# Kernel tuning notes

Hardware: AMD Instinct MI355X
Metric: run time of the kernel (lower is better)

Reference implementation:

```python
import jax, jax.numpy as jnp
import numpy as np

ALPHA = 0.25
GAMMA = 2.0
EPS = 1e-4


def calc_iou(a, b):
    # a: [A,4] anchors xyxy, b: [M,4] gt boxes xyxy -> [A,M]
    area = (b[:, 2] - b[:, 0]) * (b[:, 3] - b[:, 1])  # [M]
    iw = jnp.minimum(a[:, 2:3], b[None, :, 2]) - jnp.maximum(a[:, 0:1], b[None, :, 0])
    ih = jnp.minimum(a[:, 3:4], b[None, :, 3]) - jnp.maximum(a[:, 1:2], b[None, :, 1])
    iw = jnp.clip(iw, 0.0)
    ih = jnp.clip(ih, 0.0)
    anchor_area = ((a[:, 2] - a[:, 0]) * (a[:, 3] - a[:, 1]))[:, None]
    ua = jnp.clip(anchor_area + area[None, :] - iw * ih, 1e-8)
    return iw * ih / ua


def setup_inputs() -> dict:
    B, A, K, M = 8, 120000, 80, 32
    key = jax.random.key(0)
    k1, k2, k3, k4, k5, k6, k7 = jax.random.split(key, 7)
    classifications = jax.random.uniform(k1, (B, A, K), dtype=jnp.float32)
    regressions = jax.random.normal(k2, (B, A, 4), dtype=jnp.float32) * 0.1
    # anchors: valid xyxy boxes with positive width/height
    a_xy = jax.random.uniform(k3, (A, 2), minval=0.0, maxval=480.0)
    a_wh = jax.random.uniform(k4, (A, 2), minval=16.0, maxval=128.0)
    anchors = jnp.concatenate([a_xy, a_xy + a_wh], axis=1)[None].astype(jnp.float32)
    # annotations: [B, M, 5] valid gt boxes, labels in [0, K)
    g_xy = jax.random.uniform(k5, (B, M, 2), minval=0.0, maxval=400.0)
    g_wh = jax.random.uniform(k6, (B, M, 2), minval=20.0, maxval=120.0)
    labels = jax.random.randint(k7, (B, M, 1), 0, K).astype(jnp.float32)
    annotations = jnp.concatenate([g_xy, g_xy + g_wh, labels], axis=2).astype(jnp.float32)
    return {"classifications": classifications, "regressions": regressions,
            "anchors": anchors, "annotations": annotations}


def reference(classifications, regressions, anchors, annotations):
    anchor = anchors[0]  # [A,4]
    aw = anchor[:, 2] - anchor[:, 0]
    ah = anchor[:, 3] - anchor[:, 1]
    acx = anchor[:, 0] + 0.5 * aw
    acy = anchor[:, 1] + 0.5 * ah
    reg_scale = jnp.array([0.1, 0.1, 0.2, 0.2], dtype=classifications.dtype)

    def per_item(cls, reg, ann):
        # cls: [A,K], reg: [A,4], ann: [M,5]
        valid = ann[:, 4] != -1.0  # [M] padding mask
        c = jnp.clip(cls, EPS, 1.0 - EPS)
        iou = jnp.where(valid[None, :], calc_iou(anchor, ann[:, :4]), -1.0)  # [A,M]
        iou_max = iou.max(axis=1)
        iou_argmax = iou.argmax(axis=1)
        assigned = ann[iou_argmax]  # [A,5] gather
        pos = iou_max >= 0.5
        neg = iou_max < 0.4
        num_pos = pos.sum().astype(c.dtype)
        # targets: 1 at assigned class for positives, 0 for negatives, -1 = ignore
        onehot = jax.nn.one_hot(assigned[:, 4].astype(jnp.int32), c.shape[1], dtype=c.dtype)
        t = jnp.where(pos[:, None], onehot, jnp.where(neg[:, None], 0.0, -1.0))
        alpha_factor = jnp.where(t == 1.0, ALPHA, 1.0 - ALPHA)
        focal_weight = jnp.where(t == 1.0, 1.0 - c, c)
        bce = -(t * jnp.log(c) + (1.0 - t) * jnp.log(1.0 - c))
        cls_loss = jnp.where(t != -1.0, alpha_factor * focal_weight ** GAMMA * bce, 0.0)
        cls_loss = cls_loss.sum() / jnp.maximum(num_pos, 1.0)
        gw0 = assigned[:, 2] - assigned[:, 0]
        gh0 = assigned[:, 3] - assigned[:, 1]
        gcx = assigned[:, 0] + 0.5 * gw0
        gcy = assigned[:, 1] + 0.5 * gh0
        gw = jnp.maximum(gw0, 1.0)
        gh = jnp.maximum(gh0, 1.0)
        rt = jnp.stack([(gcx - acx) / aw, (gcy - acy) / ah,
                        jnp.log(gw / aw), jnp.log(gh / ah)], axis=1) / reg_scale
        diff = jnp.abs(rt - reg)
        smooth = jnp.where(diff <= 1.0 / 9.0, 0.5 * 9.0 * diff ** 2, diff - 0.5 / 9.0)
        reg_loss = jnp.where(num_pos > 0.0,
                             (smooth * pos[:, None]).sum() / jnp.maximum(num_pos * 4.0, 1.0),
                             0.0)
        return cls_loss, reg_loss

    cls_l, reg_l = jax.vmap(per_item)(classifications, regressions, annotations)
    return cls_l.mean(keepdims=True), reg_l.mean(keepdims=True)
```

## Files before the change

### kernel.cpp

```cpp
#include <hip/hip_runtime.h>

#define NB 8
#define NA 120000
#define NK 80
#define NM 32

#define ALPHA_F 0.25f
#define EPS_F 1e-4f

#define TPB (NA / 64)
#define BLKW 4
#define BPBW ((TPB + BLKW - 1) / BLKW)


typedef float f32x4 __attribute__((ext_vector_type(4)));

__device__ __forceinline__ f32x4 ntload4(const f32x4* p) {
    return __builtin_nontemporal_load(p);
}

__device__ __forceinline__ float clampc(float x) {
    return fminf(fmaxf(x, EPS_F), 1.0f - EPS_F);
}
__device__ __forceinline__ float negl(float c) {
    return (1.0f - ALPHA_F) * c * c * (-__logf(1.0f - c));
}
__device__ __forceinline__ float posl(float c) {
    const float omc = 1.0f - c;
    return ALPHA_F * omc * omc * (-__logf(c));
}
__device__ __forceinline__ float negl4v(f32x4 v) {
    return negl(clampc(v.x)) + negl(clampc(v.y)) + negl(clampc(v.z)) + negl(clampc(v.w));
}

__global__ __launch_bounds__(256) void fused_kernel(
    const float* __restrict__ anchors,
    const float* __restrict__ regressions,
    const float* __restrict__ annotations,
    const float* __restrict__ cls,
    float* __restrict__ part)
{
    const int b = blockIdx.x / BPBW;
    const int blk = blockIdx.x % BPBW;
    const int wid = threadIdx.x >> 6;
    const int lane = threadIdx.x & 63;
    const int tile = blk * BLKW + wid;

    __shared__ float ann[NM * 5];
    __shared__ float barea[NM];
    if (threadIdx.x < NM * 5) ann[threadIdx.x] = annotations[b * NM * 5 + threadIdx.x];
    __syncthreads();
    if (threadIdx.x < NM) {
        const float* r = &ann[threadIdx.x * 5];
        barea[threadIdx.x] = (r[2] - r[0]) * (r[3] - r[1]);
    }
    __syncthreads();

    float reg_local = 0.0f;
    float pos_local = 0.0f;
    float cls_local = 0.0f;

    if (tile < TPB) {
        const int a = tile * 64 + lane;
        float maskf = 1.0f;

        {
            const float4 av = ((const float4*)anchors)[a];
            const float aw = av.z - av.x;
            const float ah = av.w - av.y;
            const float aarea = aw * ah;

            float bi = -1.0f, bu = 1.0f;
            int bm = 0;
            #pragma unroll 4
            for (int m = 0; m < NM; ++m) {
                const float bx1 = ann[m * 5 + 0];
                const float by1 = ann[m * 5 + 1];
                const float bx2 = ann[m * 5 + 2];
                const float by2 = ann[m * 5 + 3];
                const float lbl = ann[m * 5 + 4];
                const float iw = fmaxf(fminf(av.z, bx2) - fmaxf(av.x, bx1), 0.0f);
                const float ih = fmaxf(fminf(av.w, by2) - fmaxf(av.y, by1), 0.0f);
                float inter = iw * ih;
                float ua = fmaxf(aarea + barea[m] - inter, 1e-8f);
                if (lbl == -1.0f) { inter = -1.0f; ua = 1.0f; }
                if (inter * bu > bi * ua) { bi = inter; bu = ua; bm = m; }
            }

            if (bi >= 0.5f * bu) {
                const int st = (int)ann[bm * 5 + 4];
                const float bx1 = ann[bm * 5 + 0];
                const float by1 = ann[bm * 5 + 1];
                const float bx2 = ann[bm * 5 + 2];
                const float by2 = ann[bm * 5 + 3];
                const float gw0 = bx2 - bx1;
                const float gh0 = by2 - by1;
                const float gcx = bx1 + 0.5f * gw0;
                const float gcy = by1 + 0.5f * gh0;
                const float gw = fmaxf(gw0, 1.0f);
                const float gh = fmaxf(gh0, 1.0f);
                const float acx = av.x + 0.5f * aw;
                const float acy = av.y + 0.5f * ah;
                const float rt0 = ((gcx - acx) / aw) / 0.1f;
                const float rt1 = ((gcy - acy) / ah) / 0.1f;
                const float rt2 = logf(gw / aw) / 0.2f;
                const float rt3 = logf(gh / ah) / 0.2f;
                const float4 rg = ((const float4*)regressions)[b * NA + a];
                float s = 0.0f, d;
                d = fabsf(rt0 - rg.x); s += (d <= 1.0f / 9.0f) ? 4.5f * d * d : d - 0.5f / 9.0f;
                d = fabsf(rt1 - rg.y); s += (d <= 1.0f / 9.0f) ? 4.5f * d * d : d - 0.5f / 9.0f;
                d = fabsf(rt2 - rg.z); s += (d <= 1.0f / 9.0f) ? 4.5f * d * d : d - 0.5f / 9.0f;
                d = fabsf(rt3 - rg.w); s += (d <= 1.0f / 9.0f) ? 4.5f * d * d : d - 0.5f / 9.0f;
                reg_local = s;
                pos_local = 1.0f;
                const float c = clampc(cls[((size_t)b * NA + a) * NK + st]);
                cls_local = posl(c) - negl(c);
            } else if (bi >= 0.4f * bu) {
                maskf = 0.0f;
            }
        }

        unsigned long long ig = __ballot(maskf == 0.0f);

        const f32x4* __restrict__ p =
            (const f32x4*)(cls + ((size_t)b * NA + (size_t)tile * 64) * NK);
        float sum = 0.0f;
        #pragma unroll
        for (int o = 0; o < 4; ++o) {
            f32x4 v[5];
            #pragma unroll
            for (int u = 0; u < 5; ++u)
                v[u] = ntload4(p + (o * 5 + u) * 64 + lane);
            #pragma unroll
            for (int u = 0; u < 5; ++u)
                sum += negl4v(v[u]);
        }

        while (ig) {
            const int r = __ffsll(ig) - 1;
            ig &= ig - 1;
            if (lane < 20)
                sum -= negl4v(ntload4(p + r * 20 + lane));
        }
        cls_local += sum;
    }

    #pragma unroll
    for (int o = 32; o > 0; o >>= 1) {
        cls_local += __shfl_down(cls_local, o, 64);
        reg_local += __shfl_down(reg_local, o, 64);
        pos_local += __shfl_down(pos_local, o, 64);
    }
    __shared__ float wc[BLKW], wr[BLKW], wp[BLKW];
    if (lane == 0) { wc[wid] = cls_local; wr[wid] = reg_local; wp[wid] = pos_local; }
    __syncthreads();
    if (threadIdx.x == 0) {
        float csum = 0.0f, rsum = 0.0f, psum = 0.0f;
        #pragma unroll
        for (int i = 0; i < BLKW; ++i) { csum += wc[i]; rsum += wr[i]; psum += wp[i]; }
        float4 o4;
        o4.x = csum; o4.y = rsum; o4.z = psum; o4.w = 0.0f;
        ((float4*)part)[blockIdx.x] = o4;
    }
}

__global__ __launch_bounds__(512) void finalize_kernel(
    const float* __restrict__ part,
    float* __restrict__ out)
{
    __shared__ float redC[NB], redR[NB], redP[NB];
    const int w = threadIdx.x >> 6;
    const int lane = threadIdx.x & 63;

    float c = 0.0f, r = 0.0f, p = 0.0f;
    #pragma unroll
    for (int u = 0; u < 8; ++u) {
        const int i = u * 64 + lane;
        if (i < BPBW) {
            const float4 q = ((const float4*)part)[w * BPBW + i];
            c += q.x; r += q.y; p += q.z;
        }
    }
    #pragma unroll
    for (int o = 32; o > 0; o >>= 1) {
        c += __shfl_down(c, o, 64);
        r += __shfl_down(r, o, 64);
        p += __shfl_down(p, o, 64);
    }
    if (lane == 0) { redC[w] = c; redR[w] = r; redP[w] = p; }
    __syncthreads();
    if (threadIdx.x == 0) {
        float cs = 0.0f, rs = 0.0f;
        #pragma unroll
        for (int b = 0; b < NB; ++b) {
            const float P = redP[b];
            cs += redC[b] / fmaxf(P, 1.0f);
            rs += (P > 0.0f) ? redR[b] / fmaxf(P * 4.0f, 1.0f) : 0.0f;
        }
        out[0] = cs / (float)NB;
        out[1] = rs / (float)NB;
    }
}

extern "C" void kernel_launch(void* const* d_in, const int* in_sizes, int n_in,
                              void* d_out, int out_size, void* d_ws, size_t ws_size,
                              hipStream_t stream) {
    const float* cls = (const float*)d_in[0];
    const float* reg = (const float*)d_in[1];
    const float* anc = (const float*)d_in[2];
    const float* ann = (const float*)d_in[3];

    float* part = (float*)d_ws;
    float* out = (float*)d_out;

    fused_kernel<<<NB * BPBW, 256, 0, stream>>>(anc, reg, ann, cls, part);
    finalize_kernel<<<1, 512, 0, stream>>>(part, out);
}
```

Measured before the change: 75.60 us.

## Split fused kernel into separate anchor-assignment and classification-streaming kernels

Splits the single fused kernel into an assignment kernel and a streaming kernel. The assignment kernel computes IoU matching, the positive-anchor losses and a per-anchor ignore mask written to workspace. The streaming kernel reads that mask and streams the classification tensor for the negative focal-loss sum. The intent is to take the IoU compute off the bandwidth-bound streaming path so its loads can issue immediately. The cost is an extra kernel launch and a mask write and read through global memory.

```diff
diff --git a/kernel.cpp b/kernel.cpp
--- a/kernel.cpp
+++ b/kernel.cpp
@@ -12,6 +12,8 @@
 #define BLKW 4
 #define BPBW ((TPB + BLKW - 1) / BLKW)
 
+#define PART_A_OFF (4u << 20)
+#define PART_S_OFF ((4u << 20) + (64u << 10))
 
 typedef float f32x4 __attribute__((ext_vector_type(4)));
 
@@ -33,12 +35,13 @@
     return negl(clampc(v.x)) + negl(clampc(v.y)) + negl(clampc(v.z)) + negl(clampc(v.w));
 }
 
-__global__ __launch_bounds__(256) void fused_kernel(
+__global__ __launch_bounds__(256) void assign_kernel(
     const float* __restrict__ anchors,
     const float* __restrict__ regressions,
     const float* __restrict__ annotations,
     const float* __restrict__ cls,
-    float* __restrict__ part)
+    float* __restrict__ mask,
+    float* __restrict__ part_a)
 {
     const int b = blockIdx.x / BPBW;
     const int blk = blockIdx.x % BPBW;
@@ -64,67 +67,100 @@
         const int a = tile * 64 + lane;
         float maskf = 1.0f;
 
-        {
-            const float4 av = ((const float4*)anchors)[a];
-            const float aw = av.z - av.x;
-            const float ah = av.w - av.y;
-            const float aarea = aw * ah;
-
-            float bi = -1.0f, bu = 1.0f;
-            int bm = 0;
-            #pragma unroll 4
-            for (int m = 0; m < NM; ++m) {
-                const float bx1 = ann[m * 5 + 0];
-                const float by1 = ann[m * 5 + 1];
-                const float bx2 = ann[m * 5 + 2];
-                const float by2 = ann[m * 5 + 3];
-                const float lbl = ann[m * 5 + 4];
-                const float iw = fmaxf(fminf(av.z, bx2) - fmaxf(av.x, bx1), 0.0f);
-                const float ih = fmaxf(fminf(av.w, by2) - fmaxf(av.y, by1), 0.0f);
-                float inter = iw * ih;
-                float ua = fmaxf(aarea + barea[m] - inter, 1e-8f);
-                if (lbl == -1.0f) { inter = -1.0f; ua = 1.0f; }
-                if (inter * bu > bi * ua) { bi = inter; bu = ua; bm = m; }
-            }
-
-            if (bi >= 0.5f * bu) {
-                const int st = (int)ann[bm * 5 + 4];
-                const float bx1 = ann[bm * 5 + 0];
-                const float by1 = ann[bm * 5 + 1];
-                const float bx2 = ann[bm * 5 + 2];
-                const float by2 = ann[bm * 5 + 3];
-                const float gw0 = bx2 - bx1;
-                const float gh0 = by2 - by1;
-                const float gcx = bx1 + 0.5f * gw0;
-                const float gcy = by1 + 0.5f * gh0;
-                const float gw = fmaxf(gw0, 1.0f);
-                const float gh = fmaxf(gh0, 1.0f);
-                const float acx = av.x + 0.5f * aw;
-                const float acy = av.y + 0.5f * ah;
-                const float rt0 = ((gcx - acx) / aw) / 0.1f;
-                const float rt1 = ((gcy - acy) / ah) / 0.1f;
-                const float rt2 = logf(gw / aw) / 0.2f;
-                const float rt3 = logf(gh / ah) / 0.2f;
-                const float4 rg = ((const float4*)regressions)[b * NA + a];
-                float s = 0.0f, d;
-                d = fabsf(rt0 - rg.x); s += (d <= 1.0f / 9.0f) ? 4.5f * d * d : d - 0.5f / 9.0f;
-                d = fabsf(rt1 - rg.y); s += (d <= 1.0f / 9.0f) ? 4.5f * d * d : d - 0.5f / 9.0f;
-                d = fabsf(rt2 - rg.z); s += (d <= 1.0f / 9.0f) ? 4.5f * d * d : d - 0.5f / 9.0f;
-                d = fabsf(rt3 - rg.w); s += (d <= 1.0f / 9.0f) ? 4.5f * d * d : d - 0.5f / 9.0f;
-                reg_local = s;
-                pos_local = 1.0f;
-                const float c = clampc(cls[((size_t)b * NA + a) * NK + st]);
-                cls_local = posl(c) - negl(c);
-            } else if (bi >= 0.4f * bu) {
-                maskf = 0.0f;
-            }
-        }
-
-        unsigned long long ig = __ballot(maskf == 0.0f);
+        const float4 av = ((const float4*)anchors)[a];
+        const float aw = av.z - av.x;
+        const float ah = av.w - av.y;
+        const float aarea = aw * ah;
+
+        float bi = -1.0f, bu = 1.0f;
+        int bm = 0;
+        #pragma unroll 4
+        for (int m = 0; m < NM; ++m) {
+            const float bx1 = ann[m * 5 + 0];
+            const float by1 = ann[m * 5 + 1];
+            const float bx2 = ann[m * 5 + 2];
+            const float by2 = ann[m * 5 + 3];
+            const float lbl = ann[m * 5 + 4];
+            const float iw = fmaxf(fminf(av.z, bx2) - fmaxf(av.x, bx1), 0.0f);
+            const float ih = fmaxf(fminf(av.w, by2) - fmaxf(av.y, by1), 0.0f);
+            float inter = iw * ih;
+            float ua = fmaxf(aarea + barea[m] - inter, 1e-8f);
+            if (lbl == -1.0f) { inter = -1.0f; ua = 1.0f; }
+            if (inter * bu > bi * ua) { bi = inter; bu = ua; bm = m; }
+        }
+
+        if (bi >= 0.5f * bu) {
+            const int st = (int)ann[bm * 5 + 4];
+            const float bx1 = ann[bm * 5 + 0];
+            const float by1 = ann[bm * 5 + 1];
+            const float bx2 = ann[bm * 5 + 2];
+            const float by2 = ann[bm * 5 + 3];
+            const float gw0 = bx2 - bx1;
+            const float gh0 = by2 - by1;
+            const float gcx = bx1 + 0.5f * gw0;
+            const float gcy = by1 + 0.5f * gh0;
+            const float gw = fmaxf(gw0, 1.0f);
+            const float gh = fmaxf(gh0, 1.0f);
+            const float acx = av.x + 0.5f * aw;
+            const float acy = av.y + 0.5f * ah;
+            const float rt0 = ((gcx - acx) / aw) / 0.1f;
+            const float rt1 = ((gcy - acy) / ah) / 0.1f;
+            const float rt2 = logf(gw / aw) / 0.2f;
+            const float rt3 = logf(gh / ah) / 0.2f;
+            const float4 rg = ((const float4*)regressions)[b * NA + a];
+            float s = 0.0f, d;
+            d = fabsf(rt0 - rg.x); s += (d <= 1.0f / 9.0f) ? 4.5f * d * d : d - 0.5f / 9.0f;
+            d = fabsf(rt1 - rg.y); s += (d <= 1.0f / 9.0f) ? 4.5f * d * d : d - 0.5f / 9.0f;
+            d = fabsf(rt2 - rg.z); s += (d <= 1.0f / 9.0f) ? 4.5f * d * d : d - 0.5f / 9.0f;
+            d = fabsf(rt3 - rg.w); s += (d <= 1.0f / 9.0f) ? 4.5f * d * d : d - 0.5f / 9.0f;
+            reg_local = s;
+            pos_local = 1.0f;
+            const float c = clampc(cls[((size_t)b * NA + a) * NK + st]);
+            cls_local = posl(c) - negl(c);
+        } else if (bi >= 0.4f * bu) {
+            maskf = 0.0f;
+        }
+        mask[b * NA + a] = maskf;
+    }
+
+    #pragma unroll
+    for (int o = 32; o > 0; o >>= 1) {
+        cls_local += __shfl_down(cls_local, o, 64);
+        reg_local += __shfl_down(reg_local, o, 64);
+        pos_local += __shfl_down(pos_local, o, 64);
+    }
+    __shared__ float wc[BLKW], wr[BLKW], wp[BLKW];
+    if (lane == 0) { wc[wid] = cls_local; wr[wid] = reg_local; wp[wid] = pos_local; }
+    __syncthreads();
+    if (threadIdx.x == 0) {
+        float csum = 0.0f, rsum = 0.0f, psum = 0.0f;
+        #pragma unroll
+        for (int i = 0; i < BLKW; ++i) { csum += wc[i]; rsum += wr[i]; psum += wp[i]; }
+        float4 o4;
+        o4.x = csum; o4.y = rsum; o4.z = psum; o4.w = 0.0f;
+        ((float4*)part_a)[blockIdx.x] = o4;
+    }
+}
+
+__global__ __launch_bounds__(256) void stream_kernel(
+    const float* __restrict__ mask,
+    const float* __restrict__ cls,
+    float* __restrict__ part_s)
+{
+    const int b = blockIdx.x / BPBW;
+    const int blk = blockIdx.x % BPBW;
+    const int wid = threadIdx.x >> 6;
+    const int lane = threadIdx.x & 63;
+    const int tile = blk * BLKW + wid;
+
+    float sum = 0.0f;
+
+    if (tile < TPB) {
+        const float maskf = mask[b * NA + tile * 64 + lane];
+        const unsigned long long ig = __ballot(maskf == 0.0f);
 
         const f32x4* __restrict__ p =
             (const f32x4*)(cls + ((size_t)b * NA + (size_t)tile * 64) * NK);
-        float sum = 0.0f;
         #pragma unroll
         for (int o = 0; o < 4; ++o) {
             f32x4 v[5];
@@ -136,36 +172,31 @@
                 sum += negl4v(v[u]);
         }
 
-        while (ig) {
-            const int r = __ffsll(ig) - 1;
-            ig &= ig - 1;
+        unsigned long long w = ig;
+        while (w) {
+            const int r = __ffsll(w) - 1;
+            w &= w - 1;
             if (lane < 20)
                 sum -= negl4v(ntload4(p + r * 20 + lane));
         }
-        cls_local += sum;
-    }
-
-    #pragma unroll
-    for (int o = 32; o > 0; o >>= 1) {
-        cls_local += __shfl_down(cls_local, o, 64);
-        reg_local += __shfl_down(reg_local, o, 64);
-        pos_local += __shfl_down(pos_local, o, 64);
-    }
-    __shared__ float wc[BLKW], wr[BLKW], wp[BLKW];
-    if (lane == 0) { wc[wid] = cls_local; wr[wid] = reg_local; wp[wid] = pos_local; }
+    }
+
+    #pragma unroll
+    for (int o = 32; o > 0; o >>= 1) sum += __shfl_down(sum, o, 64);
+    __shared__ float ws[BLKW];
+    if (lane == 0) ws[wid] = sum;
     __syncthreads();
     if (threadIdx.x == 0) {
-        float csum = 0.0f, rsum = 0.0f, psum = 0.0f;
-        #pragma unroll
-        for (int i = 0; i < BLKW; ++i) { csum += wc[i]; rsum += wr[i]; psum += wp[i]; }
-        float4 o4;
-        o4.x = csum; o4.y = rsum; o4.z = psum; o4.w = 0.0f;
-        ((float4*)part)[blockIdx.x] = o4;
+        float s = 0.0f;
+        #pragma unroll
+        for (int i = 0; i < BLKW; ++i) s += ws[i];
+        part_s[blockIdx.x] = s;
     }
 }
 
 __global__ __launch_bounds__(512) void finalize_kernel(
-    const float* __restrict__ part,
+    const float* __restrict__ part_s,
+    const float* __restrict__ part_a,
     float* __restrict__ out)
 {
     __shared__ float redC[NB], redR[NB], redP[NB];
@@ -177,7 +208,8 @@
     for (int u = 0; u < 8; ++u) {
         const int i = u * 64 + lane;
         if (i < BPBW) {
-            const float4 q = ((const float4*)part)[w * BPBW + i];
+            c += part_s[w * BPBW + i];
+            const float4 q = ((const float4*)part_a)[w * BPBW + i];
             c += q.x; r += q.y; p += q.z;
         }
     }
@@ -210,9 +242,12 @@
     const float* anc = (const float*)d_in[2];
     const float* ann = (const float*)d_in[3];
 
-    float* part = (float*)d_ws;
+    float* mask   = (float*)d_ws;
+    float* part_a = (float*)((char*)d_ws + PART_A_OFF);
+    float* part_s = (float*)((char*)d_ws + PART_S_OFF);
     float* out = (float*)d_out;
 
-    fused_kernel<<<NB * BPBW, 256, 0, stream>>>(anc, reg, ann, cls, part);
-    finalize_kernel<<<1, 512, 0, stream>>>(part, out);
-}
+    assign_kernel<<<NB * BPBW, 256, 0, stream>>>(anc, reg, ann, cls, mask, part_a);
+    stream_kernel<<<NB * BPBW, 256, 0, stream>>>(mask, cls, part_s);
+    finalize_kernel<<<1, 512, 0, stream>>>(part_s, part_a, out);
+}
```

After: 89.98 us. 1.19x slower.
